# Kernel optimization log

Measured on AMD Instinct MI355X. Metric: run time of the kernel, lower is better.

Reference implementation:

```python
import jax, jax.numpy as jnp
import numpy as np

H, HD, CHUNK = 16, 64, 128


def _rotary(x):
    # x: (B,H,N,d); rotary_embedding_torch default: interleaved pairs, theta=10000
    N, d = x.shape[-2], x.shape[-1]
    inv_freq = 1.0 / (10000.0 ** (jnp.arange(0, d, 2, dtype=jnp.float32) / d))
    ang = jnp.arange(N, dtype=jnp.float32)[:, None] * inv_freq[None, :]  # (N, d/2)
    ang = jnp.repeat(ang, 2, axis=-1)  # (N, d), each freq repeated twice
    cos, sin = jnp.cos(ang), jnp.sin(ang)
    x1, x2 = x[..., 0::2], x[..., 1::2]
    xr = jnp.stack([-x2, x1], axis=-1).reshape(x.shape)  # rotate_half (interleaved)
    return x * cos + xr * sin


def _split_heads(t, B, N):
    return t.reshape(B, N, H, HD).transpose(0, 2, 1, 3)  # (B,H,N,Hd)


def _chunked(Q, KK, VK):
    # chunk-parallel linear-attention recurrence: per-token outer products,
    # intra-chunk cumsum, carried state across chunks, Frobenius normalization.
    B, h, N, d = Q.shape
    nc = N // CHUNK

    def to_chunks(t):
        return t.reshape(B, h, nc, CHUNK, d).transpose(2, 0, 1, 3, 4)  # (nc,B,h,c,d)

    S0 = jnp.eye(d, dtype=Q.dtype) * jnp.sqrt(jnp.float32(d))
    S0 = jnp.broadcast_to(S0, (B, h, d, d))

    def step(SK_state, inp):
        q, kk, vk = inp  # (B,h,c,d)
        ok = jnp.einsum('bhni,bhnj->bhnij', kk, vk)            # outer products
        SK = jnp.cumsum(ok, axis=2) + SK_state[:, :, None]      # prefix-sum + carry
        norm = jnp.sqrt(jnp.sum(SK * SK, axis=(-2, -1), keepdims=True)) + 1e-8
        SKn = SK / norm                                         # Frobenius-normalized
        y = jnp.einsum('bhni,bhnji->bhnj', q, SKn)              # q @ SK^T per token
        return SK[:, :, -1], y

    _, ys = jax.lax.scan(step, S0, (to_chunks(Q), to_chunks(KK), to_chunks(VK)))
    return ys.transpose(1, 2, 0, 3, 4).reshape(B, h, N, d)


def setup_inputs():
    key = jax.random.key(0)
    ks = jax.random.split(key, 5)
    B, N, D = 2, 2048, 1024
    X = jax.random.normal(ks[0], (B, N, D), jnp.float32)
    w_qkv = jax.random.normal(ks[1], (D, 3 * H * HD), jnp.float32) * 0.02
    w_kvkv = jax.random.normal(ks[2], (D, 4 * H * HD), jnp.float32) * 0.02
    w_out = jax.random.normal(ks[3], (H * HD, D), jnp.float32) * 0.02
    b_out = jnp.zeros((D,), jnp.float32)
    return {"X": X, "w_qkv": w_qkv, "w_kvkv": w_kvkv, "w_out": w_out, "b_out": b_out}


def reference(X, w_qkv, w_kvkv, w_out, b_out):
    B, N, D = X.shape
    q, k, v = jnp.split(X @ w_qkv, 3, axis=-1)
    Q = _split_heads(q, B, N)
    K = _split_heads(k, B, N)
    V = _split_heads(v, B, N)
    kk, vk, _kv, _vv = jnp.split(X @ w_kvkv, 4, axis=-1)
    KK = _split_heads(kk, B, N)
    VK = _split_heads(vk, B, N)
    # NOTE: the SV branch (KV, VV) in the original is returned by the chunked fn
    # but never used by forward's output, so it is dead code for the fwd result.
    Qn = _chunked(Q, KK, VK)
    Qr = _rotary(Qn)
    Kr = _rotary(K)
    scale = 1.0 / jnp.sqrt(jnp.float32(HD))
    scores = jnp.einsum('bhqd,bhkd->bhqk', Qr, Kr) * scale
    mask = jnp.tril(jnp.ones((N, N), dtype=bool))
    scores = jnp.where(mask, scores, -jnp.inf)
    attn = jax.nn.softmax(scores, axis=-1)
    out = jnp.einsum('bhqk,bhkd->bhqd', attn, V)
    out = out.transpose(0, 2, 1, 3).reshape(B, N, H * HD)
    return out @ w_out + b_out
```

## Files before the change

### kernel.cpp

```cpp
#include <hip/hip_runtime.h>

typedef unsigned int u32;
typedef unsigned short u16;
typedef __attribute__((ext_vector_type(8))) __bf16 bf16x8;
typedef __attribute__((ext_vector_type(4))) float f32x4;

constexpr int NH = 16;
constexpr int HDM = 64;
constexpr int NSQ = 2048;
constexpr int KD = 1024;
constexpr int BHT = 32;
constexpr float ROT_C = 13.287712379549449f / 32.0f;

__device__ __forceinline__ u16 f2bf(float f) {
  u32 u = __float_as_uint(f);
  u += 0x7fffu + ((u >> 16) & 1u);
  return (u16)(u >> 16);
}
__device__ __forceinline__ float bf2f(u16 h) {
  return __uint_as_float(((u32)h) << 16);
}

__device__ __forceinline__ void fast_sincos(float th, float* s, float* c) {
  __sincosf(th, s, c);
}

__device__ __forceinline__ void gl_lds16(const u16* g, u16* l) {
  __builtin_amdgcn_global_load_lds(
      (const __attribute__((address_space(1))) u32*)g,
      (__attribute__((address_space(3))) u32*)l, 16, 0, 0);
}

__device__ __forceinline__ bf16x8 ldf(const u16* b, int row, int cb, int rs) {
  return *(const bf16x8*)((const char*)b + row * rs + ((cb * 16) ^ ((row & 7) << 4)));
}

__global__ void k_f32_to_bf16(const float* __restrict__ src, u16* __restrict__ dst, int n4) {
  int i = blockIdx.x * 256 + threadIdx.x;
  if (i < n4) {
    float4 v = ((const float4*)src)[i];
    ushort4 o;
    o.x = f2bf(v.x); o.y = f2bf(v.y); o.z = f2bf(v.z); o.w = f2bf(v.w);
    ((ushort4*)dst)[i] = o;
  }
}

__global__ void k_transpose_bf16(const float* __restrict__ src, int srcld,
                                 u16* __restrict__ dst, int dstld) {
  __shared__ float tile[64][65];
  int ct = blockIdx.x * 64, kt = blockIdx.y * 64;
  int lc = threadIdx.x & 63, rg = threadIdx.x >> 6;
#pragma unroll
  for (int i = 0; i < 16; ++i) {
    int kl = rg * 16 + i;
    tile[kl][lc] = src[(size_t)(kt + kl) * srcld + ct + lc];
  }
  __syncthreads();
#pragma unroll
  for (int i = 0; i < 16; ++i) {
    int cl = rg * 16 + i;
    dst[(size_t)(ct + cl) * dstld + kt + lc] = f2bf(tile[lc][cl]);
  }
}

__device__ __forceinline__ void stage_v3(const u16* __restrict__ gA, const u16* __restrict__ gB,
                                         u16* AL, u16* BL, int mb, int nb, int kt, int tid) {
#pragma unroll
  for (int l = 0; l < 2; ++l) {
    int i = tid + l * 512;
    int row = i >> 3, cb = i & 7;
    int col = (cb ^ (row & 7)) << 3;
    gl_lds16(gA + (size_t)(mb + row) * KD + kt * 64 + col, AL + i * 8);
  }
#pragma unroll
  for (int l = 0; l < 4; ++l) {
    int i = tid + l * 512;
    int row = i >> 3, cb = i & 7;
    int col = (cb ^ (row & 7)) << 3;
    gl_lds16(gB + (size_t)(nb + row) * KD + kt * 64 + col, BL + i * 8);
  }
}

__device__ __forceinline__ void compute_v3(const u16* AL, const u16* BL,
                                           f32x4 (&acc)[4][4], int wr, int wc, int g, int q) {
#pragma unroll
  for (int ks = 0; ks < 2; ++ks) {
    bf16x8 af[4], bfr[4];
#pragma unroll
    for (int nf = 0; nf < 4; ++nf)
      bfr[nf] = ldf(BL, wc * 64 + nf * 16 + q, ks * 4 + g, 128);
#pragma unroll
    for (int mf = 0; mf < 4; ++mf)
      af[mf] = ldf(AL, wr * 64 + mf * 16 + q, ks * 4 + g, 128);
    __builtin_amdgcn_s_setprio(1);
#pragma unroll
    for (int mf = 0; mf < 4; ++mf)
#pragma unroll
      for (int nf = 0; nf < 4; ++nf)
        acc[mf][nf] = __builtin_amdgcn_mfma_f32_16x16x32_bf16(af[mf], bfr[nf], acc[mf][nf], 0, 0, 0);
    __builtin_amdgcn_s_setprio(0);
  }
}

__global__ __launch_bounds__(512) void k_gemm0_v3(const u16* __restrict__ A,
                                                  const u16* __restrict__ Bt,
                                                  u16* __restrict__ o0, u16* __restrict__ o1,
                                                  u16* __restrict__ o2, u16* __restrict__ o3,
                                                  u16* __restrict__ o4) {
  __shared__ __align__(16) u16 AL[2][8192];
  __shared__ __align__(16) u16 BL[2][16384];
  int bid = blockIdx.x;
  int swz = (bid & 7) * 80 + (bid >> 3);
  int nt = swz % 20, mt = swz / 20;
  int tid = threadIdx.x, w = tid >> 6, lane = tid & 63;
  int g = lane >> 4, q = lane & 15;
  int wr = w >> 2, wc = w & 3;
  int mb = mt * 128, nb = nt * 256;

  f32x4 acc[4][4];
#pragma unroll
  for (int m = 0; m < 4; ++m)
#pragma unroll
    for (int n = 0; n < 4; ++n) acc[m][n] = (f32x4){0.f, 0.f, 0.f, 0.f};

  stage_v3(A, Bt, AL[0], BL[0], mb, nb, 0, tid);
  stage_v3(A, Bt, AL[1], BL[1], mb, nb, 1, tid);
  asm volatile("s_waitcnt vmcnt(6)" ::: "memory");
  asm volatile("s_barrier" ::: "memory");
  __builtin_amdgcn_sched_barrier(0);

#define GBODY(KT, PBUF)                                                     \
  {                                                                         \
    compute_v3(AL[PBUF], BL[PBUF], acc, wr, wc, g, q);                      \
    asm volatile("s_barrier" ::: "memory");                                 \
    if ((KT) + 2 < 16) {                                                    \
      stage_v3(A, Bt, AL[PBUF], BL[PBUF], mb, nb, (KT) + 2, tid);           \
      asm volatile("s_waitcnt vmcnt(6)" ::: "memory");                      \
    } else if ((KT) == 14) {                                                \
      asm volatile("s_waitcnt vmcnt(0)" ::: "memory");                      \
    }                                                                       \
    asm volatile("s_barrier" ::: "memory");                                 \
    __builtin_amdgcn_sched_barrier(0);                                      \
  }

  for (int it = 0; it < 8; ++it) {
    GBODY(2 * it, 0);
    GBODY(2 * it + 1, 1);
  }
#undef GBODY

#pragma unroll
  for (int nf = 0; nf < 4; ++nf) {
    int c = nt * 256 + wc * 64 + nf * 16 + q;
    int t = c >> 10;
    if (t == 1) {
      int rem = c & 1023;
      int hh = rem >> 6, dd = rem & 63;
      float invf = exp2f(-(float)(dd >> 1) * ROT_C);
      float sgn = (dd & 1) ? 1.0f : -1.0f;
      size_t hoff = (size_t)hh * NSQ * HDM + dd;
#pragma unroll
      for (int mf = 0; mf < 4; ++mf)
#pragma unroll
        for (int r = 0; r < 4; ++r) {
          int row = mt * 128 + wr * 64 + mf * 16 + g * 4 + r;
          int b = row >> 11, nn = row & 2047;
          float mine = acc[mf][nf][r];
          float part = __shfl_xor(mine, 1);
          float s, cc;
          fast_sincos((float)nn * invf, &s, &cc);
          o1[(size_t)b * NH * NSQ * HDM + hoff + (size_t)nn * HDM] = f2bf(mine * cc + sgn * part * s);
        }
    } else if (t == 2) {
      int rem = c & 1023;
      int hh = rem >> 6, dd = rem & 63;
#pragma unroll
      for (int mf = 0; mf < 4; ++mf)
#pragma unroll
        for (int r = 0; r < 4; ++r) {
          int row = mt * 128 + wr * 64 + mf * 16 + g * 4 + r;
          int b = row >> 11, nn = row & 2047;
          o2[((size_t)(b * NH + hh) * HDM + dd) * NSQ + nn] = f2bf(acc[mf][nf][r]);
        }
    } else {
      u16* dst = (t == 0) ? o0 : ((t == 3) ? o3 : o4);
      int rem = c & 1023;
      size_t hoff = (size_t)(rem >> 6) * NSQ * HDM + (rem & 63);
#pragma unroll
      for (int mf = 0; mf < 4; ++mf)
#pragma unroll
        for (int r = 0; r < 4; ++r) {
          int row = mt * 128 + wr * 64 + mf * 16 + g * 4 + r;
          int b = row >> 11, nn = row & 2047;
          dst[(size_t)b * NH * NSQ * HDM + hoff + (size_t)nn * HDM] = f2bf(acc[mf][nf][r]);
        }
    }
  }
}

__device__ __forceinline__ void gemm_stage_o(const u16* __restrict__ A, const u16* __restrict__ Bt,
                                             u16* Albuf, u16* Blbuf, int mt, int nt, int kt,
                                             int tid) {
  {
    int i = tid;
    int row = i >> 2;
    int ke = (i & 3) * 8;
    int grow = mt * 64 + row;
    int k = kt * 32 + ke;
    const u16* ga = A + ((size_t)((grow >> 11) * NH + (k >> 6)) * NSQ + (grow & 2047)) * HDM + (k & 63);
    gl_lds16(ga, Albuf + i * 8);
  }
#pragma unroll
  for (int l = 0; l < 2; ++l) {
    int i = tid + l * 256;
    int row = i >> 2;
    int ke = (i & 3) * 8;
    const u16* gb = Bt + (size_t)(nt * 128 + row) * KD + kt * 32 + ke;
    gl_lds16(gb, Blbuf + i * 8);
  }
}

__device__ __forceinline__ void gemm_compute_o(const u16* Albuf, const u16* Blbuf,
                                               f32x4 acc[2][4], int wr, int wc, int g, int q) {
  bf16x8 af[2], bfr[4];
#pragma unroll
  for (int m = 0; m < 2; ++m)
    af[m] = *(const bf16x8*)(Albuf + (wr * 32 + m * 16 + q) * 32 + g * 8);
#pragma unroll
  for (int n = 0; n < 4; ++n)
    bfr[n] = *(const bf16x8*)(Blbuf + (wc * 64 + n * 16 + q) * 32 + g * 8);
#pragma unroll
  for (int m = 0; m < 2; ++m)
#pragma unroll
    for (int n = 0; n < 4; ++n)
      acc[m][n] = __builtin_amdgcn_mfma_f32_16x16x32_bf16(af[m], bfr[n], acc[m][n], 0, 0, 0);
}

__global__ __launch_bounds__(256) void k_gemm_out(const u16* __restrict__ A, const u16* __restrict__ Bt,
                                                  const float* __restrict__ bias,
                                                  float* __restrict__ Cout) {
  __shared__ __align__(16) u16 Al[2][2048];
  __shared__ __align__(16) u16 Bl[2][4096];
  int nt = blockIdx.x, mt = blockIdx.y;
  int tid = threadIdx.x, w = tid >> 6, lane = tid & 63;
  int g = lane >> 4, q = lane & 15, wr = w >> 1, wc = w & 1;
  f32x4 acc[2][4];
#pragma unroll
  for (int m = 0; m < 2; ++m)
#pragma unroll
    for (int n = 0; n < 4; ++n) acc[m][n] = (f32x4){0.f, 0.f, 0.f, 0.f};

  gemm_stage_o(A, Bt, Al[0], Bl[0], mt, nt, 0, tid);
  __syncthreads();
  int cur = 0;
  for (int kt = 1; kt < 32; ++kt) {
    gemm_stage_o(A, Bt, Al[cur ^ 1], Bl[cur ^ 1], mt, nt, kt, tid);
    gemm_compute_o(Al[cur], Bl[cur], acc, wr, wc, g, q);
    __syncthreads();
    cur ^= 1;
  }
  gemm_compute_o(Al[cur], Bl[cur], acc, wr, wc, g, q);

#pragma unroll
  for (int nf = 0; nf < 4; ++nf) {
    int c = nt * 128 + wc * 64 + nf * 16 + q;
    float bv = bias[c];
#pragma unroll
    for (int mf = 0; mf < 2; ++mf)
#pragma unroll
      for (int r = 0; r < 4; ++r) {
        int row = mt * 64 + wr * 32 + mf * 16 + g * 4 + r;
        Cout[(size_t)row * 1024 + c] = acc[mf][nf][r] + bv;
      }
  }
}

__global__ __launch_bounds__(256) void k_chunk_outer(const u16* __restrict__ Kk,
                                                     const u16* __restrict__ Vk,
                                                     float* __restrict__ Mc) {
  int bhc = blockIdx.x;
  __shared__ float kk[128][64];
  __shared__ float vv[128][64];
  int tid = threadIdx.x;
  size_t base = ((size_t)(bhc >> 4) * NSQ + (size_t)(bhc & 15) * 128) * HDM;
  for (int i = tid; i < 2048; i += 256) {
    int r = i >> 4, c4 = (i & 15) * 4;
    ushort4 a = ((const ushort4*)(Kk + base))[i];
    kk[r][c4] = bf2f(a.x); kk[r][c4 + 1] = bf2f(a.y); kk[r][c4 + 2] = bf2f(a.z); kk[r][c4 + 3] = bf2f(a.w);
    ushort4 b = ((const ushort4*)(Vk + base))[i];
    vv[r][c4] = bf2f(b.x); vv[r][c4 + 1] = bf2f(b.y); vv[r][c4 + 2] = bf2f(b.z); vv[r][c4 + 3] = bf2f(b.w);
  }
  __syncthreads();
  int i0 = (tid >> 4) * 4, j0 = (tid & 15) * 4;
  float a2[4][4];
#pragma unroll
  for (int di = 0; di < 4; ++di)
#pragma unroll
    for (int dj = 0; dj < 4; ++dj) a2[di][dj] = 0.f;
  for (int m = 0; m < 128; ++m) {
    float ka[4], vb[4];
#pragma unroll
    for (int d = 0; d < 4; ++d) { ka[d] = kk[m][i0 + d]; vb[d] = vv[m][j0 + d]; }
#pragma unroll
    for (int di = 0; di < 4; ++di)
#pragma unroll
      for (int dj = 0; dj < 4; ++dj) a2[di][dj] += ka[di] * vb[dj];
  }
  float* out = Mc + (size_t)bhc * 4096;
#pragma unroll
  for (int di = 0; di < 4; ++di) {
    float4 v = make_float4(a2[di][0], a2[di][1], a2[di][2], a2[di][3]);
    *(float4*)(out + (i0 + di) * 64 + j0) = v;
  }
}

__global__ __launch_bounds__(256) void k_chunk_prefix2(const float* __restrict__ Mc,
                                                       float* __restrict__ Sst) {
  int bh = blockIdx.x, rg = blockIdx.y;
  int tid = threadIdx.x;
  int r8 = tid >> 5, cp = tid & 31;
  int i = rg * 8 + r8, j0 = cp * 2;
  float s0 = (i == j0) ? 8.0f : 0.0f;
  float s1 = (i == j0 + 1) ? 8.0f : 0.0f;
  size_t rowoff = (size_t)i * 64 + j0;
  for (int c = 0; c < 16; ++c) {
    size_t o = ((size_t)bh * 16 + c) * 4096 + rowoff;
    *(float2*)(Sst + o) = make_float2(s0, s1);
    float2 mv = *(const float2*)(Mc + o);
    s0 += mv.x; s1 += mv.y;
  }
}

__global__ __launch_bounds__(256) void k_chunk_norm(const u16* __restrict__ Kk,
                                                    const u16* __restrict__ Vk,
                                                    const float* __restrict__ Sst,
                                                    float* __restrict__ Invn) {
  __shared__ __align__(16) u16 KkL[128 * 64];
  __shared__ __align__(16) u16 VkL[128 * 64];
  __shared__ __align__(16) u16 SL[64 * 64];
  __shared__ float prebuf[128][2];
  __shared__ float bilbuf[128][2];
  __shared__ float sc[128];
  __shared__ float red[4];
  int bhc = blockIdx.x;
  int tid = threadIdx.x, w = tid >> 6, lane = tid & 63;
  int g = lane >> 4, q = lane & 15;
  size_t base = (size_t)bhc * 8192;

  for (int ic = tid; ic < 1024; ic += 256) {
    int row = ic >> 3, cb = ic & 7;
    int off = row * 128 + ((cb * 16) ^ ((row & 7) << 4));
    *(uint4*)((char*)KkL + off) = ((const uint4*)(Kk + base))[ic];
    *(uint4*)((char*)VkL + off) = ((const uint4*)(Vk + base))[ic];
  }
  float ss = 0.f;
  const float4* Sg = (const float4*)(Sst + (size_t)bhc * 4096);
  for (int i = tid; i < 1024; i += 256) {
    float4 v = Sg[i];
    ss += v.x * v.x + v.y * v.y + v.z * v.z + v.w * v.w;
    int row = i >> 4, c8 = (i & 15) * 8;
    u32 lo = (u32)f2bf(v.x) | ((u32)f2bf(v.y) << 16);
    u32 hi = (u32)f2bf(v.z) | ((u32)f2bf(v.w) << 16);
    *(uint2*)((char*)SL + row * 128 + (c8 ^ ((row & 7) << 4))) = make_uint2(lo, hi);
  }
#pragma unroll
  for (int d = 1; d < 64; d <<= 1) ss += __shfl_xor(ss, d);
  if (lane == 0) red[w] = ss;
  __syncthreads();

  int wr = w >> 1, wc = w & 1;
  bf16x8 ka[4][2], va[4][2];
#pragma unroll
  for (int mf = 0; mf < 4; ++mf)
#pragma unroll
    for (int ks = 0; ks < 2; ++ks) {
      ka[mf][ks] = ldf(KkL, wr * 64 + mf * 16 + q, ks * 4 + g, 128);
      va[mf][ks] = ldf(VkL, wr * 64 + mf * 16 + q, ks * 4 + g, 128);
    }

  float pracc[4][4];
#pragma unroll
  for (int mf = 0; mf < 4; ++mf)
#pragma unroll
    for (int r = 0; r < 4; ++r) pracc[mf][r] = 0.f;
  for (int pf = 0; pf < 4; ++pf) {
    bf16x8 kb0 = ldf(KkL, wc * 64 + pf * 16 + q, g, 128);
    bf16x8 kb1 = ldf(KkL, wc * 64 + pf * 16 + q, 4 + g, 128);
    bf16x8 vb0 = ldf(VkL, wc * 64 + pf * 16 + q, g, 128);
    bf16x8 vb1 = ldf(VkL, wc * 64 + pf * 16 + q, 4 + g, 128);
#pragma unroll
    for (int mf = 0; mf < 4; ++mf) {
      f32x4 a1 = (f32x4){0.f, 0.f, 0.f, 0.f}, b1 = (f32x4){0.f, 0.f, 0.f, 0.f};
      a1 = __builtin_amdgcn_mfma_f32_16x16x32_bf16(ka[mf][0], kb0, a1, 0, 0, 0);
      a1 = __builtin_amdgcn_mfma_f32_16x16x32_bf16(ka[mf][1], kb1, a1, 0, 0, 0);
      b1 = __builtin_amdgcn_mfma_f32_16x16x32_bf16(va[mf][0], vb0, b1, 0, 0, 0);
      b1 = __builtin_amdgcn_mfma_f32_16x16x32_bf16(va[mf][1], vb1, b1, 0, 0, 0);
#pragma unroll
      for (int r = 0; r < 4; ++r) {
        int m = wr * 64 + mf * 16 + g * 4 + r;
        int p = wc * 64 + pf * 16 + q;
        float gv = a1[r] * b1[r];
        float coef = (p < m) ? 1.f : ((p == m) ? 0.5f : 0.f);
        pracc[mf][r] += coef * gv;
      }
    }
  }
#pragma unroll
  for (int mf = 0; mf < 4; ++mf)
#pragma unroll
    for (int r = 0; r < 4; ++r) {
      float v = pracc[mf][r];
      v += __shfl_xor(v, 1); v += __shfl_xor(v, 2); v += __shfl_xor(v, 4); v += __shfl_xor(v, 8);
      pracc[mf][r] = v;
    }
  if (q == 0) {
#pragma unroll
    for (int mf = 0; mf < 4; ++mf)
#pragma unroll
      for (int r = 0; r < 4; ++r) prebuf[wr * 64 + mf * 16 + g * 4 + r][wc] = pracc[mf][r];
  }

  float bacc[4][4];
#pragma unroll
  for (int mf = 0; mf < 4; ++mf)
#pragma unroll
    for (int r = 0; r < 4; ++r) bacc[mf][r] = 0.f;
  for (int jf = 0; jf < 2; ++jf) {
    bf16x8 sb0 = ldf(SL, wc * 32 + jf * 16 + q, g, 128);
    bf16x8 sb1 = ldf(SL, wc * 32 + jf * 16 + q, 4 + g, 128);
#pragma unroll
    for (int mf = 0; mf < 4; ++mf) {
      f32x4 u = (f32x4){0.f, 0.f, 0.f, 0.f};
      u = __builtin_amdgcn_mfma_f32_16x16x32_bf16(va[mf][0], sb0, u, 0, 0, 0);
      u = __builtin_amdgcn_mfma_f32_16x16x32_bf16(va[mf][1], sb1, u, 0, 0, 0);
#pragma unroll
      for (int r = 0; r < 4; ++r) {
        int m = wr * 64 + mf * 16 + g * 4 + r;
        int j = wc * 32 + jf * 16 + q;
        float kkv = bf2f(*(const u16*)((const char*)KkL + m * 128 + ((j * 2) ^ ((m & 7) << 4))));
        bacc[mf][r] += u[r] * kkv;
      }
    }
  }
#pragma unroll
  for (int mf = 0; mf < 4; ++mf)
#pragma unroll
    for (int r = 0; r < 4; ++r) {
      float v = bacc[mf][r];
      v += __shfl_xor(v, 1); v += __shfl_xor(v, 2); v += __shfl_xor(v, 4); v += __shfl_xor(v, 8);
      bacc[mf][r] = v;
    }
  if (q == 0) {
#pragma unroll
    for (int mf = 0; mf < 4; ++mf)
#pragma unroll
      for (int r = 0; r < 4; ++r) bilbuf[wr * 64 + mf * 16 + g * 4 + r][wc] = bacc[mf][r];
  }
  __syncthreads();

  if (tid < 128)
    sc[tid] = 2.f * (prebuf[tid][0] + prebuf[tid][1] + bilbuf[tid][0] + bilbuf[tid][1]);
  __syncthreads();
  for (int off = 1; off < 128; off <<= 1) {
    float add = 0.f;
    if (tid < 128 && tid >= off) add = sc[tid - off];
    __syncthreads();
    if (tid < 128) sc[tid] += add;
    __syncthreads();
  }
  if (tid < 128) {
    float n0 = red[0] + red[1] + red[2] + red[3];
    float cum = n0 + sc[tid];
    Invn[(size_t)bhc * 128 + tid] = 1.f / (sqrtf(cum) + 1e-8f);
  }
}

__global__ __launch_bounds__(256) void k_chunk_yv2(const u16* __restrict__ Qb,
                                                   const u16* __restrict__ Kk,
                                                   const u16* __restrict__ Vk,
                                                   const float* __restrict__ Sst,
                                                   const float* __restrict__ Invn,
                                                   u16* __restrict__ Qro) {
  __shared__ __align__(16) u16 QL[128 * 64];
  __shared__ __align__(16) u16 WL[128 * 64];
  __shared__ __align__(16) u16 SL[64 * 64];
  __shared__ __align__(16) u16 PL[128 * 128];
  __shared__ float inv[128];
  int bhc = blockIdx.x;
  int tid = threadIdx.x, w = tid >> 6, lane = tid & 63;
  int g = lane >> 4, q = lane & 15;
  size_t base = (size_t)bhc * 8192;

  for (int ic = tid; ic < 1024; ic += 256) {
    int row = ic >> 3, cb = ic & 7;
    int off = row * 128 + ((cb * 16) ^ ((row & 7) << 4));
    *(uint4*)((char*)QL + off) = ((const uint4*)(Qb + base))[ic];
    *(uint4*)((char*)WL + off) = ((const uint4*)(Vk + base))[ic];
  }
  const float4* Sg = (const float4*)(Sst + (size_t)bhc * 4096);
  for (int i = tid; i < 1024; i += 256) {
    float4 v = Sg[i];
    int row = i >> 4, c8 = (i & 15) * 8;
    u32 lo = (u32)f2bf(v.x) | ((u32)f2bf(v.y) << 16);
    u32 hi = (u32)f2bf(v.z) | ((u32)f2bf(v.w) << 16);
    *(uint2*)((char*)SL + row * 128 + (c8 ^ ((row & 7) << 4))) = make_uint2(lo, hi);
  }
  if (tid < 128) inv[tid] = Invn[(size_t)bhc * 128 + tid];
  __syncthreads();

  int wr = w >> 1, wc = w & 1;
  f32x4 pacc[4][4];
#pragma unroll
  for (int mf = 0; mf < 4; ++mf)
#pragma unroll
    for (int nf = 0; nf < 4; ++nf) pacc[mf][nf] = (f32x4){0.f, 0.f, 0.f, 0.f};
#pragma unroll
  for (int ks = 0; ks < 2; ++ks) {
    bf16x8 av[4], bq[4];
#pragma unroll
    for (int mf = 0; mf < 4; ++mf) av[mf] = ldf(WL, wr * 64 + mf * 16 + q, ks * 4 + g, 128);
#pragma unroll
    for (int nf = 0; nf < 4; ++nf) bq[nf] = ldf(QL, wc * 64 + nf * 16 + q, ks * 4 + g, 128);
#pragma unroll
    for (int mf = 0; mf < 4; ++mf)
#pragma unroll
      for (int nf = 0; nf < 4; ++nf)
        pacc[mf][nf] = __builtin_amdgcn_mfma_f32_16x16x32_bf16(av[mf], bq[nf], pacc[mf][nf], 0, 0, 0);
  }
#pragma unroll
  for (int mf = 0; mf < 4; ++mf)
#pragma unroll
    for (int nf = 0; nf < 4; ++nf) {
      int m0 = wr * 64 + mf * 16 + g * 4;
      int n = wc * 64 + nf * 16 + q;
      float v0 = (m0 + 0 <= n) ? pacc[mf][nf][0] : 0.f;
      float v1 = (m0 + 1 <= n) ? pacc[mf][nf][1] : 0.f;
      float v2 = (m0 + 2 <= n) ? pacc[mf][nf][2] : 0.f;
      float v3 = (m0 + 3 <= n) ? pacc[mf][nf][3] : 0.f;
      u32 lo = (u32)f2bf(v0) | ((u32)f2bf(v1) << 16);
      u32 hi = (u32)f2bf(v2) | ((u32)f2bf(v3) << 16);
      *(uint2*)((char*)PL + n * 256 + ((m0 * 2) ^ ((n & 7) << 4))) = make_uint2(lo, hi);
    }
  __syncthreads();
  for (int i = tid; i < 2048; i += 256) {
    int r = i >> 4, c4 = (i & 15) * 4;
    ushort4 kv = ((const ushort4*)(Kk + base))[i];
    *(u16*)((char*)WL + (c4 + 0) * 256 + ((r * 2) ^ (((c4 + 0) & 7) << 4))) = kv.x;
    *(u16*)((char*)WL + (c4 + 1) * 256 + ((r * 2) ^ (((c4 + 1) & 7) << 4))) = kv.y;
    *(u16*)((char*)WL + (c4 + 2) * 256 + ((r * 2) ^ (((c4 + 2) & 7) << 4))) = kv.z;
    *(u16*)((char*)WL + (c4 + 3) * 256 + ((r * 2) ^ (((c4 + 3) & 7) << 4))) = kv.w;
  }
  __syncthreads();

  f32x4 yacc[4][2];
#pragma unroll
  for (int nf = 0; nf < 4; ++nf)
#pragma unroll
    for (int jf = 0; jf < 2; ++jf) yacc[nf][jf] = (f32x4){0.f, 0.f, 0.f, 0.f};
#pragma unroll
  for (int ks = 0; ks < 2; ++ks) {
    bf16x8 aq[4], bs[2];
#pragma unroll
    for (int nf = 0; nf < 4; ++nf) aq[nf] = ldf(QL, wr * 64 + nf * 16 + q, ks * 4 + g, 128);
#pragma unroll
    for (int jf = 0; jf < 2; ++jf) bs[jf] = ldf(SL, wc * 32 + jf * 16 + q, ks * 4 + g, 128);
#pragma unroll
    for (int nf = 0; nf < 4; ++nf)
#pragma unroll
      for (int jf = 0; jf < 2; ++jf)
        yacc[nf][jf] = __builtin_amdgcn_mfma_f32_16x16x32_bf16(aq[nf], bs[jf], yacc[nf][jf], 0, 0, 0);
  }
#pragma unroll
  for (int ks = 0; ks < 4; ++ks) {
    bf16x8 ap[4], bk[2];
#pragma unroll
    for (int nf = 0; nf < 4; ++nf) ap[nf] = ldf(PL, wr * 64 + nf * 16 + q, ks * 4 + g, 256);
#pragma unroll
    for (int jf = 0; jf < 2; ++jf) bk[jf] = ldf(WL, wc * 32 + jf * 16 + q, ks * 4 + g, 256);
#pragma unroll
    for (int nf = 0; nf < 4; ++nf)
#pragma unroll
      for (int jf = 0; jf < 2; ++jf)
        yacc[nf][jf] = __builtin_amdgcn_mfma_f32_16x16x32_bf16(ap[nf], bk[jf], yacc[nf][jf], 0, 0, 0);
  }
#pragma unroll
  for (int nf = 0; nf < 4; ++nf)
#pragma unroll
    for (int jf = 0; jf < 2; ++jf) {
      int j = wc * 32 + jf * 16 + q;
      float invf = exp2f(-(float)(j >> 1) * ROT_C);
      float sgn = (j & 1) ? 1.0f : -1.0f;
#pragma unroll
      for (int r = 0; r < 4; ++r) {
        int n = wr * 64 + nf * 16 + g * 4 + r;
        float val = yacc[nf][jf][r] * inv[n];
        float part = __shfl_xor(val, 1);
        int ng = (bhc & 15) * 128 + n;
        float s, cc;
        fast_sincos((float)ng * invf, &s, &cc);
        Qro[base + (size_t)n * 64 + j] = f2bf((val * cc + sgn * part * s) * 0.125f);
      }
    }
}

__global__ __launch_bounds__(512) void k_attn3(const u16* __restrict__ Qr, const u16* __restrict__ Kr,
                                               const u16* __restrict__ Vt, u16* __restrict__ Ob) {
  __shared__ __align__(16) u16 QL[128 * 64];
  __shared__ __align__(16) u16 KL[2][64 * 64];
  __shared__ __align__(16) u16 VL[2][64 * 64];
  __shared__ __align__(16) u16 PLa[8][16 * 64];
  int bh = blockIdx.x, pair = blockIdx.y, phase = blockIdx.z;
  int tid = threadIdx.x, w = tid >> 6, lane = tid & 63;
  int g = lane >> 4, q16 = lane & 15;
  const u16* Qg_base = Qr + (size_t)bh * NSQ * HDM;
  const u16* Kg_base = Kr + (size_t)bh * NSQ * HDM;
  const u16* VTg_base = Vt + (size_t)bh * HDM * NSQ;
  u16* Og_base = Ob + (size_t)bh * NSQ * HDM;
  u16* Pw = PLa[w];
  int srow = tid >> 3, scb = tid & 7;

  int t = phase ? (15 - pair) : pair;
  int qbase = t * 128;
  int nkt = 2 * t + 2;
  int lastkt_w = (qbase + w * 16 + 15) >> 6;
  int qg_ = qbase + w * 16 + q16;

  {
    const u16* Qg = Qg_base + qbase * 64;
#pragma unroll
    for (int it = 0; it < 2; ++it) {
      int c = it * 512 + tid;
      int row = c >> 3, cb = c & 7;
      gl_lds16(Qg + row * 64 + ((cb ^ (row & 7)) << 3), QL + c * 8);
    }
  }
  gl_lds16(Kg_base + srow * 64 + ((scb ^ (srow & 7)) << 3), KL[0] + tid * 8);
  gl_lds16(VTg_base + (size_t)srow * NSQ + ((scb ^ (srow & 7)) << 3), VL[0] + tid * 8);
  __syncthreads();

  bf16x8 qf[2];
  qf[0] = ldf(QL, w * 16 + q16, g, 128);
  qf[1] = ldf(QL, w * 16 + q16, 4 + g, 128);

  f32x4 o[4];
#pragma unroll
  for (int df = 0; df < 4; ++df) o[df] = (f32x4){0.f, 0.f, 0.f, 0.f};
  float m_run = -3.0e38f, l_run = 0.f;

  int cur = 0;
  for (int kt = 0; kt < nkt; ++kt) {
    if (kt + 1 < nkt) {
      gl_lds16(Kg_base + (kt + 1) * 4096 + srow * 64 + ((scb ^ (srow & 7)) << 3),
               KL[cur ^ 1] + tid * 8);
      gl_lds16(VTg_base + (size_t)srow * NSQ + (kt + 1) * 64 + ((scb ^ (srow & 7)) << 3),
               VL[cur ^ 1] + tid * 8);
    }
    if (kt <= lastkt_w) {
      const u16* Kbuf = KL[cur];
      const u16* Vbuf = VL[cur];
      f32x4 st[4];
#pragma unroll
      for (int kf = 0; kf < 4; ++kf) {
        f32x4 s = (f32x4){0.f, 0.f, 0.f, 0.f};
        s = __builtin_amdgcn_mfma_f32_16x16x32_bf16(ldf(Kbuf, kf * 16 + q16, g, 128), qf[0], s, 0, 0, 0);
        s = __builtin_amdgcn_mfma_f32_16x16x32_bf16(ldf(Kbuf, kf * 16 + q16, 4 + g, 128), qf[1], s, 0, 0, 0);
        st[kf] = s;
      }
      float smax = -1e30f;
      bool needmask = (kt * 64 + 63 > qbase + w * 16);
      if (needmask) {
#pragma unroll
        for (int kf = 0; kf < 4; ++kf)
#pragma unroll
          for (int r = 0; r < 4; ++r) {
            int keyg = kt * 64 + kf * 16 + g * 4 + r;
            float sv = st[kf][r];
            sv = (keyg <= qg_) ? sv : -1e30f;
            st[kf][r] = sv;
            smax = fmaxf(smax, sv);
          }
      } else {
#pragma unroll
        for (int kf = 0; kf < 4; ++kf)
#pragma unroll
          for (int r = 0; r < 4; ++r) smax = fmaxf(smax, st[kf][r]);
      }
      smax = fmaxf(smax, __shfl_xor(smax, 16));
      smax = fmaxf(smax, __shfl_xor(smax, 32));
      float mnew = fmaxf(m_run, smax);
      float corr = __expf(m_run - mnew);
      float ls = 0.f;
#pragma unroll
      for (int kf = 0; kf < 4; ++kf)
#pragma unroll
        for (int r = 0; r < 4; ++r) {
          float p = __expf(st[kf][r] - mnew);
          st[kf][r] = p;
          ls += p;
        }
      ls += __shfl_xor(ls, 16);
      ls += __shfl_xor(ls, 32);
      m_run = mnew;
      l_run = l_run * corr + ls;
#pragma unroll
      for (int df = 0; df < 4; ++df) {
        o[df][0] *= corr; o[df][1] *= corr; o[df][2] *= corr; o[df][3] *= corr;
      }
#pragma unroll
      for (int kf = 0; kf < 4; ++kf) {
        u32 lo = (u32)f2bf(st[kf][0]) | ((u32)f2bf(st[kf][1]) << 16);
        u32 hi = (u32)f2bf(st[kf][2]) | ((u32)f2bf(st[kf][3]) << 16);
        int ba = q16 * 128 + ((kf * 32 + g * 8) ^ ((q16 & 7) << 4));
        *(u32*)((char*)Pw + ba) = lo;
        *(u32*)((char*)Pw + ba + 4) = hi;
      }
#pragma unroll
      for (int kc = 0; kc < 2; ++kc) {
        bf16x8 pf = ldf(Pw, q16, kc * 4 + g, 128);
#pragma unroll
        for (int df = 0; df < 4; ++df) {
          bf16x8 vf = ldf(Vbuf, df * 16 + q16, kc * 4 + g, 128);
          o[df] = __builtin_amdgcn_mfma_f32_16x16x32_bf16(vf, pf, o[df], 0, 0, 0);
        }
      }
    }
    __syncthreads();
    cur ^= 1;
  }
  float invl = 1.0f / l_run;
  u16* Og = Og_base + (size_t)(qbase + w * 16 + q16) * HDM;
#pragma unroll
  for (int df = 0; df < 4; ++df)
#pragma unroll
    for (int r = 0; r < 4; ++r) Og[df * 16 + g * 4 + r] = f2bf(o[df][r] * invl);
}

extern "C" void kernel_launch(void* const* d_in, const int* in_sizes, int n_in,
                              void* d_out, int out_size, void* d_ws, size_t ws_size,
                              hipStream_t stream) {
  const float* X = (const float*)d_in[0];
  const float* w_qkv = (const float*)d_in[1];
  const float* w_kvkv = (const float*)d_in[2];
  const float* w_out = (const float*)d_in[3];
  const float* b_out = (const float*)d_in[4];
  float* out = (float*)d_out;
  char* ws = (char*)d_ws;

  u16* Xb  = (u16*)(ws + 0);
  u16* WbT = (u16*)(ws + 8388608);
  u16* WoT = (u16*)(ws + 18874368);
  u16* Qb  = (u16*)(ws + 20971520);
  float* Sst = (float*)(ws + 29360128);
  u16* Vtb = (u16*)(ws + 37748736);
  u16* Kkb = (u16*)(ws + 46137344);
  u16* Vkb = (u16*)(ws + 54525952);
  u16* Kr  = (u16*)(ws + 62914560);
  u16* Qr  = (u16*)(ws + 71303168);
  float* Mc   = (float*)(ws + 8388608);
  float* Invn = (float*)(ws + 16777216);
  u16* Ob = (u16*)(ws + 0);
  (void)in_sizes; (void)n_in; (void)out_size; (void)ws_size;

  k_f32_to_bf16<<<dim3(4096), dim3(256), 0, stream>>>(X, Xb, 1048576);
  k_transpose_bf16<<<dim3(48, 16), dim3(256), 0, stream>>>(w_qkv, 3072, WbT, 1024);
  k_transpose_bf16<<<dim3(32, 16), dim3(256), 0, stream>>>(w_kvkv, 4096, WbT + (size_t)3072 * 1024, 1024);
  k_transpose_bf16<<<dim3(16, 16), dim3(256), 0, stream>>>(w_out, 1024, WoT, 1024);
  k_gemm0_v3<<<dim3(640), dim3(512), 0, stream>>>(Xb, WbT, Qb, Kr, Vtb, Kkb, Vkb);
  k_chunk_outer<<<dim3(512), dim3(256), 0, stream>>>(Kkb, Vkb, Mc);
  k_chunk_prefix2<<<dim3(32, 8), dim3(256), 0, stream>>>(Mc, Sst);
  k_chunk_norm<<<dim3(512), dim3(256), 0, stream>>>(Kkb, Vkb, Sst, Invn);
  k_chunk_yv2<<<dim3(512), dim3(256), 0, stream>>>(Qb, Kkb, Vkb, Sst, Invn, Qr);
  k_attn3<<<dim3(32, 8, 2), dim3(512), 0, stream>>>(Qr, Kr, Vtb, Ob);
  k_gemm_out<<<dim3(8, 64), dim3(256), 0, stream>>>(Ob, WoT, b_out, out);
}
```

Measured before the change: 187.7 us.

## Fuse chunk prefix, norm and output kernels; merge weight transposes into one launch

New measurement: 195.0 us. 3.9% more time.

```diff
diff --git a/kernel.cpp b/kernel.cpp
--- a/kernel.cpp
+++ b/kernel.cpp
@@ -45,10 +45,15 @@
   }
 }
 
-__global__ void k_transpose_bf16(const float* __restrict__ src, int srcld,
-                                 u16* __restrict__ dst, int dstld) {
+__global__ void k_transpose3(const float* __restrict__ s0, const float* __restrict__ s1,
+                             const float* __restrict__ s2, u16* __restrict__ d0,
+                             u16* __restrict__ d1, u16* __restrict__ d2) {
   __shared__ float tile[64][65];
-  int ct = blockIdx.x * 64, kt = blockIdx.y * 64;
+  int bx = blockIdx.x, kt = blockIdx.y * 64;
+  const float* src; u16* dst; int srcld, ct;
+  if (bx < 48)      { src = s0; dst = d0; srcld = 3072; ct = bx * 64; }
+  else if (bx < 80) { src = s1; dst = d1; srcld = 4096; ct = (bx - 48) * 64; }
+  else              { src = s2; dst = d2; srcld = 1024; ct = (bx - 80) * 64; }
   int lc = threadIdx.x & 63, rg = threadIdx.x >> 6;
 #pragma unroll
   for (int i = 0; i < 16; ++i) {
@@ -59,7 +64,7 @@
 #pragma unroll
   for (int i = 0; i < 16; ++i) {
     int cl = rg * 16 + i;
-    dst[(size_t)(ct + cl) * dstld + kt + lc] = f2bf(tile[lc][cl]);
+    dst[(size_t)(ct + cl) * 1024 + kt + lc] = f2bf(tile[lc][cl]);
   }
 }
 
@@ -314,35 +319,23 @@
   }
 }
 
-__global__ __launch_bounds__(256) void k_chunk_prefix2(const float* __restrict__ Mc,
-                                                       float* __restrict__ Sst) {
-  int bh = blockIdx.x, rg = blockIdx.y;
-  int tid = threadIdx.x;
-  int r8 = tid >> 5, cp = tid & 31;
-  int i = rg * 8 + r8, j0 = cp * 2;
-  float s0 = (i == j0) ? 8.0f : 0.0f;
-  float s1 = (i == j0 + 1) ? 8.0f : 0.0f;
-  size_t rowoff = (size_t)i * 64 + j0;
-  for (int c = 0; c < 16; ++c) {
-    size_t o = ((size_t)bh * 16 + c) * 4096 + rowoff;
-    *(float2*)(Sst + o) = make_float2(s0, s1);
-    float2 mv = *(const float2*)(Mc + o);
-    s0 += mv.x; s1 += mv.y;
-  }
-}
-
-__global__ __launch_bounds__(256) void k_chunk_norm(const u16* __restrict__ Kk,
-                                                    const u16* __restrict__ Vk,
-                                                    const float* __restrict__ Sst,
-                                                    float* __restrict__ Invn) {
+__global__ __launch_bounds__(256) void k_chunk_fused(const u16* __restrict__ Qb,
+                                                     const u16* __restrict__ Kk,
+                                                     const u16* __restrict__ Vk,
+                                                     const float* __restrict__ Mc,
+                                                     u16* __restrict__ Qro) {
   __shared__ __align__(16) u16 KkL[128 * 64];
   __shared__ __align__(16) u16 VkL[128 * 64];
+  __shared__ __align__(16) u16 QL[128 * 64];
   __shared__ __align__(16) u16 SL[64 * 64];
+  __shared__ __align__(16) u16 PL[128 * 128];
   __shared__ float prebuf[128][2];
   __shared__ float bilbuf[128][2];
   __shared__ float sc[128];
   __shared__ float red[4];
+  __shared__ float inv[128];
   int bhc = blockIdx.x;
+  int bh = bhc >> 4, c = bhc & 15;
   int tid = threadIdx.x, w = tid >> 6, lane = tid & 63;
   int g = lane >> 4, q = lane & 15;
   size_t base = (size_t)bhc * 8192;
@@ -352,15 +345,32 @@
     int off = row * 128 + ((cb * 16) ^ ((row & 7) << 4));
     *(uint4*)((char*)KkL + off) = ((const uint4*)(Kk + base))[ic];
     *(uint4*)((char*)VkL + off) = ((const uint4*)(Vk + base))[ic];
+    *(uint4*)((char*)QL + off) = ((const uint4*)(Qb + base))[ic];
+  }
+  float s4[4][4];
+#pragma unroll
+  for (int l = 0; l < 4; ++l) {
+    int i = tid + l * 256;
+    int row = i >> 4, c4 = (i & 15) * 4;
+#pragma unroll
+    for (int j = 0; j < 4; ++j) s4[l][j] = (row == c4 + j) ? 8.0f : 0.0f;
+  }
+  for (int cc = 0; cc < c; ++cc) {
+    const float4* Mg = (const float4*)(Mc + ((size_t)bh * 16 + cc) * 4096);
+#pragma unroll
+    for (int l = 0; l < 4; ++l) {
+      float4 v = Mg[tid + l * 256];
+      s4[l][0] += v.x; s4[l][1] += v.y; s4[l][2] += v.z; s4[l][3] += v.w;
+    }
   }
   float ss = 0.f;
-  const float4* Sg = (const float4*)(Sst + (size_t)bhc * 4096);
-  for (int i = tid; i < 1024; i += 256) {
-    float4 v = Sg[i];
-    ss += v.x * v.x + v.y * v.y + v.z * v.z + v.w * v.w;
+#pragma unroll
+  for (int l = 0; l < 4; ++l) {
+    int i = tid + l * 256;
     int row = i >> 4, c8 = (i & 15) * 8;
-    u32 lo = (u32)f2bf(v.x) | ((u32)f2bf(v.y) << 16);
-    u32 hi = (u32)f2bf(v.z) | ((u32)f2bf(v.w) << 16);
+    ss += s4[l][0] * s4[l][0] + s4[l][1] * s4[l][1] + s4[l][2] * s4[l][2] + s4[l][3] * s4[l][3];
+    u32 lo = (u32)f2bf(s4[l][0]) | ((u32)f2bf(s4[l][1]) << 16);
+    u32 hi = (u32)f2bf(s4[l][2]) | ((u32)f2bf(s4[l][3]) << 16);
     *(uint2*)((char*)SL + row * 128 + (c8 ^ ((row & 7) << 4))) = make_uint2(lo, hi);
   }
 #pragma unroll
@@ -470,45 +480,9 @@
   }
   if (tid < 128) {
     float n0 = red[0] + red[1] + red[2] + red[3];
-    float cum = n0 + sc[tid];
-    Invn[(size_t)bhc * 128 + tid] = 1.f / (sqrtf(cum) + 1e-8f);
-  }
-}
-
-__global__ __launch_bounds__(256) void k_chunk_yv2(const u16* __restrict__ Qb,
-                                                   const u16* __restrict__ Kk,
-                                                   const u16* __restrict__ Vk,
-                                                   const float* __restrict__ Sst,
-                                                   const float* __restrict__ Invn,
-                                                   u16* __restrict__ Qro) {
-  __shared__ __align__(16) u16 QL[128 * 64];
-  __shared__ __align__(16) u16 WL[128 * 64];
-  __shared__ __align__(16) u16 SL[64 * 64];
-  __shared__ __align__(16) u16 PL[128 * 128];
-  __shared__ float inv[128];
-  int bhc = blockIdx.x;
-  int tid = threadIdx.x, w = tid >> 6, lane = tid & 63;
-  int g = lane >> 4, q = lane & 15;
-  size_t base = (size_t)bhc * 8192;
-
-  for (int ic = tid; ic < 1024; ic += 256) {
-    int row = ic >> 3, cb = ic & 7;
-    int off = row * 128 + ((cb * 16) ^ ((row & 7) << 4));
-    *(uint4*)((char*)QL + off) = ((const uint4*)(Qb + base))[ic];
-    *(uint4*)((char*)WL + off) = ((const uint4*)(Vk + base))[ic];
-  }
-  const float4* Sg = (const float4*)(Sst + (size_t)bhc * 4096);
-  for (int i = tid; i < 1024; i += 256) {
-    float4 v = Sg[i];
-    int row = i >> 4, c8 = (i & 15) * 8;
-    u32 lo = (u32)f2bf(v.x) | ((u32)f2bf(v.y) << 16);
-    u32 hi = (u32)f2bf(v.z) | ((u32)f2bf(v.w) << 16);
-    *(uint2*)((char*)SL + row * 128 + (c8 ^ ((row & 7) << 4))) = make_uint2(lo, hi);
-  }
-  if (tid < 128) inv[tid] = Invn[(size_t)bhc * 128 + tid];
-  __syncthreads();
-
-  int wr = w >> 1, wc = w & 1;
+    inv[tid] = 1.f / (sqrtf(n0 + sc[tid]) + 1e-8f);
+  }
+
   f32x4 pacc[4][4];
 #pragma unroll
   for (int mf = 0; mf < 4; ++mf)
@@ -516,16 +490,14 @@
     for (int nf = 0; nf < 4; ++nf) pacc[mf][nf] = (f32x4){0.f, 0.f, 0.f, 0.f};
 #pragma unroll
   for (int ks = 0; ks < 2; ++ks) {
-    bf16x8 av[4], bq[4];
-#pragma unroll
-    for (int mf = 0; mf < 4; ++mf) av[mf] = ldf(WL, wr * 64 + mf * 16 + q, ks * 4 + g, 128);
+    bf16x8 bq[4];
 #pragma unroll
     for (int nf = 0; nf < 4; ++nf) bq[nf] = ldf(QL, wc * 64 + nf * 16 + q, ks * 4 + g, 128);
 #pragma unroll
     for (int mf = 0; mf < 4; ++mf)
 #pragma unroll
       for (int nf = 0; nf < 4; ++nf)
-        pacc[mf][nf] = __builtin_amdgcn_mfma_f32_16x16x32_bf16(av[mf], bq[nf], pacc[mf][nf], 0, 0, 0);
+        pacc[mf][nf] = __builtin_amdgcn_mfma_f32_16x16x32_bf16(va[mf][ks], bq[nf], pacc[mf][nf], 0, 0, 0);
   }
 #pragma unroll
   for (int mf = 0; mf < 4; ++mf)
@@ -541,14 +513,13 @@
       u32 hi = (u32)f2bf(v2) | ((u32)f2bf(v3) << 16);
       *(uint2*)((char*)PL + n * 256 + ((m0 * 2) ^ ((n & 7) << 4))) = make_uint2(lo, hi);
     }
-  __syncthreads();
   for (int i = tid; i < 2048; i += 256) {
     int r = i >> 4, c4 = (i & 15) * 4;
     ushort4 kv = ((const ushort4*)(Kk + base))[i];
-    *(u16*)((char*)WL + (c4 + 0) * 256 + ((r * 2) ^ (((c4 + 0) & 7) << 4))) = kv.x;
-    *(u16*)((char*)WL + (c4 + 1) * 256 + ((r * 2) ^ (((c4 + 1) & 7) << 4))) = kv.y;
-    *(u16*)((char*)WL + (c4 + 2) * 256 + ((r * 2) ^ (((c4 + 2) & 7) << 4))) = kv.z;
-    *(u16*)((char*)WL + (c4 + 3) * 256 + ((r * 2) ^ (((c4 + 3) & 7) << 4))) = kv.w;
+    *(u16*)((char*)VkL + (c4 + 0) * 256 + ((r * 2) ^ (((c4 + 0) & 7) << 4))) = kv.x;
+    *(u16*)((char*)VkL + (c4 + 1) * 256 + ((r * 2) ^ (((c4 + 1) & 7) << 4))) = kv.y;
+    *(u16*)((char*)VkL + (c4 + 2) * 256 + ((r * 2) ^ (((c4 + 2) & 7) << 4))) = kv.z;
+    *(u16*)((char*)VkL + (c4 + 3) * 256 + ((r * 2) ^ (((c4 + 3) & 7) << 4))) = kv.w;
   }
   __syncthreads();
 
@@ -576,7 +547,7 @@
 #pragma unroll
     for (int nf = 0; nf < 4; ++nf) ap[nf] = ldf(PL, wr * 64 + nf * 16 + q, ks * 4 + g, 256);
 #pragma unroll
-    for (int jf = 0; jf < 2; ++jf) bk[jf] = ldf(WL, wc * 32 + jf * 16 + q, ks * 4 + g, 256);
+    for (int jf = 0; jf < 2; ++jf) bk[jf] = ldf(VkL, wc * 32 + jf * 16 + q, ks * 4 + g, 256);
 #pragma unroll
     for (int nf = 0; nf < 4; ++nf)
 #pragma unroll
@@ -595,10 +566,10 @@
         int n = wr * 64 + nf * 16 + g * 4 + r;
         float val = yacc[nf][jf][r] * inv[n];
         float part = __shfl_xor(val, 1);
-        int ng = (bhc & 15) * 128 + n;
-        float s, cc;
-        fast_sincos((float)ng * invf, &s, &cc);
-        Qro[base + (size_t)n * 64 + j] = f2bf((val * cc + sgn * part * s) * 0.125f);
+        int ng = c * 128 + n;
+        float s, cc2;
+        fast_sincos((float)ng * invf, &s, &cc2);
+        Qro[base + (size_t)n * 64 + j] = f2bf((val * cc2 + sgn * part * s) * 0.125f);
       }
     }
 }
@@ -750,26 +721,21 @@
   u16* WbT = (u16*)(ws + 8388608);
   u16* WoT = (u16*)(ws + 18874368);
   u16* Qb  = (u16*)(ws + 20971520);
-  float* Sst = (float*)(ws + 29360128);
   u16* Vtb = (u16*)(ws + 37748736);
   u16* Kkb = (u16*)(ws + 46137344);
   u16* Vkb = (u16*)(ws + 54525952);
   u16* Kr  = (u16*)(ws + 62914560);
   u16* Qr  = (u16*)(ws + 71303168);
-  float* Mc   = (float*)(ws + 8388608);
-  float* Invn = (float*)(ws + 16777216);
+  float* Mc = (float*)(ws + 8388608);
   u16* Ob = (u16*)(ws + 0);
   (void)in_sizes; (void)n_in; (void)out_size; (void)ws_size;
 
   k_f32_to_bf16<<<dim3(4096), dim3(256), 0, stream>>>(X, Xb, 1048576);
-  k_transpose_bf16<<<dim3(48, 16), dim3(256), 0, stream>>>(w_qkv, 3072, WbT, 1024);
-  k_transpose_bf16<<<dim3(32, 16), dim3(256), 0, stream>>>(w_kvkv, 4096, WbT + (size_t)3072 * 1024, 1024);
-  k_transpose_bf16<<<dim3(16, 16), dim3(256), 0, stream>>>(w_out, 1024, WoT, 1024);
+  k_transpose3<<<dim3(96, 16), dim3(256), 0, stream>>>(
+      w_qkv, w_kvkv, w_out, WbT, WbT + (size_t)3072 * 1024, WoT);
   k_gemm0_v3<<<dim3(640), dim3(512), 0, stream>>>(Xb, WbT, Qb, Kr, Vtb, Kkb, Vkb);
   k_chunk_outer<<<dim3(512), dim3(256), 0, stream>>>(Kkb, Vkb, Mc);
-  k_chunk_prefix2<<<dim3(32, 8), dim3(256), 0, stream>>>(Mc, Sst);
-  k_chunk_norm<<<dim3(512), dim3(256), 0, stream>>>(Kkb, Vkb, Sst, Invn);
-  k_chunk_yv2<<<dim3(512), dim3(256), 0, stream>>>(Qb, Kkb, Vkb, Sst, Invn, Qr);
+  k_chunk_fused<<<dim3(512), dim3(256), 0, stream>>>(Qb, Kkb, Vkb, Mc, Qr);
   k_attn3<<<dim3(32, 8, 2), dim3(512), 0, stream>>>(Qr, Kr, Vtb, Ob);
   k_gemm_out<<<dim3(8, 64), dim3(256), 0, stream>>>(Ob, WoT, b_out, out);
 }
```
